# Performance work log

Hardware: AMD Instinct MI355X
Metric: run time of the kernel (lower is better)

Reference implementation:

```python
import jax, jax.numpy as jnp
import numpy as np
import math

IN_FEATURES = 1024
OUT_FEATURES = 1024
N_BANK = 8192
N_LAYER = 12
N_EMBD = 1024


def setup_inputs() -> dict:
    key = jax.random.key(0)
    kq, kk, kv = jax.random.split(key, 3)
    q = jax.random.normal(kq, (4, 2048, IN_FEATURES), dtype=jnp.float32)
    k = 0.02 * jax.random.normal(kk, (N_BANK, IN_FEATURES), dtype=jnp.float32)
    v_std = 2.0 / N_LAYER / math.sqrt(N_EMBD)
    v = v_std * jax.random.normal(kv, (N_BANK, OUT_FEATURES), dtype=jnp.float32)
    return {"q": q, "k": k, "v": v}


def reference(q, k, v):
    # scores: [B, T, N]
    scores = jnp.einsum("btd,nd->btn", q, k)
    # row-wise L2 normalization, scaled by sqrt(N), then exact (erf) GELU
    sqrt_n = jnp.sqrt(jnp.asarray(scores.shape[-1], scores.dtype))
    norm = jnp.linalg.norm(scores, axis=-1, keepdims=True)
    gated = jax.nn.gelu(scores / norm * sqrt_n, approximate=False)
    # out: [B, T, out_features]
    return jnp.einsum("btn,no->bto", gated, v)
```

## Files before the change

### kernel.cpp

```cpp
#include <hip/hip_runtime.h>
#include <hip/hip_bf16.h>
#include <math.h>


#define MROWS 8192
#define DIN   1024
#define NBANK 8192
#define DOUT  1024

typedef float  f32x4  __attribute__((ext_vector_type(4)));
typedef __bf16 bf16x8 __attribute__((ext_vector_type(8)));

__device__ __forceinline__ float bf2f(unsigned short u) {
  union { unsigned int i; float f; } x; x.i = ((unsigned int)u) << 16; return x.f;
}
__device__ __forceinline__ unsigned short f2bf(float f) {
  union { float f; unsigned int i; } x; x.f = f;
  unsigned int u = x.i;
  unsigned int r = (u + 0x7fffu + ((u >> 16) & 1u)) >> 16;
  return (unsigned short)r;
}

__global__ void cvt_kernel(const float* __restrict__ src,
                           unsigned short* __restrict__ dst, int n) {
  int i = (blockIdx.x * 256 + threadIdx.x) * 4;
  if (i >= n) return;
  float4 vv = *(const float4*)(src + i);
  ushort4 o;
  o.x = f2bf(vv.x); o.y = f2bf(vv.y); o.z = f2bf(vv.z); o.w = f2bf(vv.w);
  *(ushort4*)(dst + i) = o;
}

__global__ void transpose_cvt_kernel(const float* __restrict__ src,
                                     unsigned short* __restrict__ dst,
                                     int R, int C) {
  __shared__ float tile[32][33];
  int c0 = blockIdx.x * 32, r0 = blockIdx.y * 32;
  for (int i = threadIdx.y; i < 32; i += 8)
    tile[i][threadIdx.x] = src[(size_t)(r0 + i) * C + c0 + threadIdx.x];
  __syncthreads();
  for (int i = threadIdx.y; i < 32; i += 8)
    dst[(size_t)(c0 + i) * R + r0 + threadIdx.x] = f2bf(tile[threadIdx.x][i]);
}

template <bool OUT_BF16>
__global__ __launch_bounds__(256, 2) void gemm_bt_kernel(
    const unsigned short* __restrict__ A, const unsigned short* __restrict__ B,
    void* __restrict__ C, int K, int ldc) {
  __shared__ unsigned short As[128 * 32];
  __shared__ unsigned short Bs[128 * 32];

  const int tid  = threadIdx.x;
  const int lane = tid & 63;
  const int wave = tid >> 6;
  const int wm   = (wave >> 1) * 64;
  const int wn   = (wave & 1) * 64;
  const int quad = lane >> 4;
  const int l16  = lane & 15;

  const size_t m0 = (size_t)blockIdx.y * 128;
  const size_t n0 = (size_t)blockIdx.x * 128;

  const int srow = tid >> 2;
  const int scol = (tid & 3) * 8;
  const unsigned short* Ag0 = A + (m0 + srow) * (size_t)K + scol;
  const unsigned short* Ag1 = A + (m0 + srow + 64) * (size_t)K + scol;
  const unsigned short* Bg0 = B + (n0 + srow) * (size_t)K + scol;
  const unsigned short* Bg1 = B + (n0 + srow + 64) * (size_t)K + scol;

  unsigned short* AsW0 = As + tid * 8;
  unsigned short* AsW1 = As + 64 * 32 + tid * 8;
  unsigned short* BsW0 = Bs + tid * 8;
  unsigned short* BsW1 = Bs + 64 * 32 + tid * 8;

  const unsigned short* ArP = As + (wm + l16) * 32 + quad * 8;
  const unsigned short* BrP = Bs + (wn + l16) * 32 + quad * 8;

  f32x4 acc[4][4];
#pragma unroll
  for (int i = 0; i < 4; i++)
#pragma unroll
    for (int j = 0; j < 4; j++) {
      f32x4 z = {0.f, 0.f, 0.f, 0.f};
      acc[i][j] = z;
    }

  for (int k0 = 0; k0 < K; k0 += 32) {
    __builtin_amdgcn_global_load_lds(
        (const __attribute__((address_space(1))) unsigned int*)(Ag0 + k0),
        (__attribute__((address_space(3))) unsigned int*)AsW0, 16, 0, 0);
    __builtin_amdgcn_global_load_lds(
        (const __attribute__((address_space(1))) unsigned int*)(Ag1 + k0),
        (__attribute__((address_space(3))) unsigned int*)AsW1, 16, 0, 0);
    __builtin_amdgcn_global_load_lds(
        (const __attribute__((address_space(1))) unsigned int*)(Bg0 + k0),
        (__attribute__((address_space(3))) unsigned int*)BsW0, 16, 0, 0);
    __builtin_amdgcn_global_load_lds(
        (const __attribute__((address_space(1))) unsigned int*)(Bg1 + k0),
        (__attribute__((address_space(3))) unsigned int*)BsW1, 16, 0, 0);
    __syncthreads();

    bf16x8 af[4], bfr[4];
#pragma unroll
    for (int i = 0; i < 4; i++) af[i] = *(const bf16x8*)(ArP + i * 16 * 32);
#pragma unroll
    for (int j = 0; j < 4; j++) bfr[j] = *(const bf16x8*)(BrP + j * 16 * 32);
#pragma unroll
    for (int i = 0; i < 4; i++)
#pragma unroll
      for (int j = 0; j < 4; j++)
        acc[i][j] = __builtin_amdgcn_mfma_f32_16x16x32_bf16(af[i], bfr[j],
                                                            acc[i][j], 0, 0, 0);
    __syncthreads();
  }

#pragma unroll
  for (int i = 0; i < 4; i++)
#pragma unroll
    for (int j = 0; j < 4; j++)
#pragma unroll
      for (int r = 0; r < 4; r++) {
        size_t row = m0 + wm + i * 16 + quad * 4 + r;
        size_t col = n0 + wn + j * 16 + l16;
        float val = acc[i][j][r];
        if (OUT_BF16)
          ((unsigned short*)C)[row * (size_t)ldc + col] = f2bf(val);
        else
          ((float*)C)[row * (size_t)ldc + col] = val;
      }
}

__global__ void rownorm_kernel(const unsigned short* __restrict__ S,
                               float* __restrict__ scale) {
  __shared__ float red[4];
  const int row = blockIdx.x;
  const unsigned short* p = S + (size_t)row * NBANK;
  float sum = 0.f;
  for (int c = threadIdx.x * 8; c < NBANK; c += 256 * 8) {
    uint4 vv = *(const uint4*)(p + c);
    unsigned int w[4] = {vv.x, vv.y, vv.z, vv.w};
#pragma unroll
    for (int e = 0; e < 4; e++) {
      float f0 = bf2f((unsigned short)(w[e] & 0xffffu));
      float f1 = bf2f((unsigned short)(w[e] >> 16));
      sum += f0 * f0 + f1 * f1;
    }
  }
#pragma unroll
  for (int off = 32; off > 0; off >>= 1) sum += __shfl_down(sum, off, 64);
  if ((threadIdx.x & 63) == 0) red[threadIdx.x >> 6] = sum;
  __syncthreads();
  if (threadIdx.x == 0) {
    float t = red[0] + red[1] + red[2] + red[3];
    scale[row] = sqrtf((float)NBANK) / sqrtf(t);
  }
}

__global__ void gelu_kernel(unsigned short* __restrict__ S,
                            const float* __restrict__ scale) {
  size_t idx = ((size_t)blockIdx.x * 256 + threadIdx.x) * 8;
  int row = (int)(idx >> 13);
  float sc = scale[row];
  uint4 vv = *(const uint4*)(S + idx);
  unsigned int w[4] = {vv.x, vv.y, vv.z, vv.w};
#pragma unroll
  for (int e = 0; e < 4; e++) {
    float x0 = bf2f((unsigned short)(w[e] & 0xffffu)) * sc;
    float x1 = bf2f((unsigned short)(w[e] >> 16)) * sc;
    float g0 = 0.5f * x0 * (1.0f + erff(x0 * 0.70710678118654752f));
    float g1 = 0.5f * x1 * (1.0f + erff(x1 * 0.70710678118654752f));
    w[e] = (unsigned int)f2bf(g0) | ((unsigned int)f2bf(g1) << 16);
  }
  uint4 o; o.x = w[0]; o.y = w[1]; o.z = w[2]; o.w = w[3];
  *(uint4*)(S + idx) = o;
}

extern "C" void kernel_launch(void* const* d_in, const int* in_sizes, int n_in,
                              void* d_out, int out_size, void* d_ws, size_t ws_size,
                              hipStream_t stream) {
  const float* q = (const float*)d_in[0];
  const float* k = (const float*)d_in[1];
  const float* v = (const float*)d_in[2];
  float* out = (float*)d_out;

  char* ws = (char*)d_ws;
  const size_t MB = 1024ull * 1024ull;
  unsigned short* qb     = (unsigned short*)(ws);
  unsigned short* kb     = (unsigned short*)(ws + 16 * MB);
  unsigned short* vbT    = (unsigned short*)(ws + 32 * MB);
  unsigned short* scores = (unsigned short*)(ws + 48 * MB);
  float*          scale  = (float*)(ws + 176 * MB);

  const int nqk = MROWS * DIN;

  cvt_kernel<<<nqk / 1024, 256, 0, stream>>>(q, qb, nqk);
  cvt_kernel<<<nqk / 1024, 256, 0, stream>>>(k, kb, nqk);
  transpose_cvt_kernel<<<dim3(DOUT / 32, NBANK / 32), dim3(32, 8), 0, stream>>>(
      v, vbT, NBANK, DOUT);

  gemm_bt_kernel<true><<<dim3(NBANK / 128, MROWS / 128), 256, 0, stream>>>(
      qb, kb, scores, DIN, NBANK);

  rownorm_kernel<<<MROWS, 256, 0, stream>>>(scores, scale);

  gelu_kernel<<<(MROWS * (size_t)NBANK) / (256 * 8), 256, 0, stream>>>(scores, scale);

  gemm_bt_kernel<false><<<dim3(DOUT / 128, MROWS / 128), 256, 0, stream>>>(
      scores, vbT, out, NBANK, DOUT);
}
```

Before: 595.2 us.

## Fuse row sum-of-squares into first GEMM and split-K second GEMM

```diff
diff --git a/kernel.cpp b/kernel.cpp
--- a/kernel.cpp
+++ b/kernel.cpp
@@ -43,12 +43,17 @@
     dst[(size_t)(c0 + i) * R + r0 + threadIdx.x] = f2bf(tile[threadIdx.x][i]);
 }
 
-template <bool OUT_BF16>
-__global__ __launch_bounds__(256, 2) void gemm_bt_kernel(
+__global__ void zero_f32_kernel(float* __restrict__ p, int n4) {
+  int i = blockIdx.x * 256 + threadIdx.x;
+  if (i < n4) ((float4*)p)[i] = make_float4(0.f, 0.f, 0.f, 0.f);
+}
+
+__global__ __launch_bounds__(256, 2) void gemm1_kernel(
     const unsigned short* __restrict__ A, const unsigned short* __restrict__ B,
-    void* __restrict__ C, int K, int ldc) {
+    unsigned short* __restrict__ C, float* __restrict__ sumsq) {
   __shared__ unsigned short As[128 * 32];
   __shared__ unsigned short Bs[128 * 32];
+  const int K = DIN, ldc = NBANK;
 
   const int tid  = threadIdx.x;
   const int lane = tid & 63;
@@ -117,43 +122,26 @@
 #pragma unroll
   for (int i = 0; i < 4; i++)
 #pragma unroll
-    for (int j = 0; j < 4; j++)
-#pragma unroll
-      for (int r = 0; r < 4; r++) {
-        size_t row = m0 + wm + i * 16 + quad * 4 + r;
-        size_t col = n0 + wn + j * 16 + l16;
+    for (int r = 0; r < 4; r++) {
+      size_t row = m0 + wm + i * 16 + quad * 4 + r;
+      float s = 0.f;
+#pragma unroll
+      for (int j = 0; j < 4; j++) {
         float val = acc[i][j][r];
-        if (OUT_BF16)
-          ((unsigned short*)C)[row * (size_t)ldc + col] = f2bf(val);
-        else
-          ((float*)C)[row * (size_t)ldc + col] = val;
+        s += val * val;
+        C[row * (size_t)ldc + n0 + wn + j * 16 + l16] = f2bf(val);
       }
-}
-
-__global__ void rownorm_kernel(const unsigned short* __restrict__ S,
-                               float* __restrict__ scale) {
-  __shared__ float red[4];
-  const int row = blockIdx.x;
-  const unsigned short* p = S + (size_t)row * NBANK;
-  float sum = 0.f;
-  for (int c = threadIdx.x * 8; c < NBANK; c += 256 * 8) {
-    uint4 vv = *(const uint4*)(p + c);
-    unsigned int w[4] = {vv.x, vv.y, vv.z, vv.w};
-#pragma unroll
-    for (int e = 0; e < 4; e++) {
-      float f0 = bf2f((unsigned short)(w[e] & 0xffffu));
-      float f1 = bf2f((unsigned short)(w[e] >> 16));
-      sum += f0 * f0 + f1 * f1;
+      s += __shfl_xor(s, 1);
+      s += __shfl_xor(s, 2);
+      s += __shfl_xor(s, 4);
+      s += __shfl_xor(s, 8);
+      if (l16 == 0) atomicAdd(&sumsq[row], s);
     }
-  }
-#pragma unroll
-  for (int off = 32; off > 0; off >>= 1) sum += __shfl_down(sum, off, 64);
-  if ((threadIdx.x & 63) == 0) red[threadIdx.x >> 6] = sum;
-  __syncthreads();
-  if (threadIdx.x == 0) {
-    float t = red[0] + red[1] + red[2] + red[3];
-    scale[row] = sqrtf((float)NBANK) / sqrtf(t);
-  }
+}
+
+__global__ void finalize_scale_kernel(float* __restrict__ s) {
+  int i = blockIdx.x * 256 + threadIdx.x;
+  if (i < MROWS) s[i] = sqrtf((float)NBANK / s[i]);
 }
 
 __global__ void gelu_kernel(unsigned short* __restrict__ S,
@@ -175,6 +163,86 @@
   *(uint4*)(S + idx) = o;
 }
 
+__global__ __launch_bounds__(512, 4) void gemm2_kernel(
+    const unsigned short* __restrict__ A,
+    const unsigned short* __restrict__ B,
+    float* __restrict__ C) {
+  __shared__ unsigned short As[128 * 32];
+  __shared__ unsigned short Bs[256 * 32];
+  const int K = NBANK, ldc = DOUT;
+
+  const int tid  = threadIdx.x;
+  const int lane = tid & 63;
+  const int wave = tid >> 6;
+  const int wm   = (wave >> 2) * 64;
+  const int wn   = (wave & 3) * 64;
+  const int quad = lane >> 4;
+  const int l16  = lane & 15;
+
+  const size_t m0 = (size_t)blockIdx.y * 128;
+  const size_t n0 = (size_t)blockIdx.x * 256;
+  const int    ks = blockIdx.z * (K / 2);
+
+  const int srow = tid >> 2;
+  const int scol = (tid & 3) * 8;
+  const unsigned short* Ag  = A + (m0 + srow) * (size_t)K + scol + ks;
+  const unsigned short* Bg0 = B + (n0 + srow) * (size_t)K + scol + ks;
+  const unsigned short* Bg1 = B + (n0 + srow + 128) * (size_t)K + scol + ks;
+
+  unsigned short* AsW  = As + tid * 8;
+  unsigned short* BsW0 = Bs + tid * 8;
+  unsigned short* BsW1 = Bs + 512 * 8 + tid * 8;
+
+  const unsigned short* ArP = As + (wm + l16) * 32 + quad * 8;
+  const unsigned short* BrP = Bs + (wn + l16) * 32 + quad * 8;
+
+  f32x4 acc[4][4];
+#pragma unroll
+  for (int i = 0; i < 4; i++)
+#pragma unroll
+    for (int j = 0; j < 4; j++) {
+      f32x4 z = {0.f, 0.f, 0.f, 0.f};
+      acc[i][j] = z;
+    }
+
+  for (int k0 = 0; k0 < K / 2; k0 += 32) {
+    __builtin_amdgcn_global_load_lds(
+        (const __attribute__((address_space(1))) unsigned int*)(Ag + k0),
+        (__attribute__((address_space(3))) unsigned int*)AsW, 16, 0, 0);
+    __builtin_amdgcn_global_load_lds(
+        (const __attribute__((address_space(1))) unsigned int*)(Bg0 + k0),
+        (__attribute__((address_space(3))) unsigned int*)BsW0, 16, 0, 0);
+    __builtin_amdgcn_global_load_lds(
+        (const __attribute__((address_space(1))) unsigned int*)(Bg1 + k0),
+        (__attribute__((address_space(3))) unsigned int*)BsW1, 16, 0, 0);
+    __syncthreads();
+
+    bf16x8 af[4], bfr[4];
+#pragma unroll
+    for (int i = 0; i < 4; i++) af[i] = *(const bf16x8*)(ArP + i * 16 * 32);
+#pragma unroll
+    for (int j = 0; j < 4; j++) bfr[j] = *(const bf16x8*)(BrP + j * 16 * 32);
+#pragma unroll
+    for (int i = 0; i < 4; i++)
+#pragma unroll
+      for (int j = 0; j < 4; j++)
+        acc[i][j] = __builtin_amdgcn_mfma_f32_16x16x32_bf16(af[i], bfr[j],
+                                                            acc[i][j], 0, 0, 0);
+    __syncthreads();
+  }
+
+#pragma unroll
+  for (int i = 0; i < 4; i++)
+#pragma unroll
+    for (int j = 0; j < 4; j++)
+#pragma unroll
+      for (int r = 0; r < 4; r++) {
+        size_t row = m0 + wm + i * 16 + quad * 4 + r;
+        size_t col = n0 + wn + j * 16 + l16;
+        atomicAdd(&C[row * (size_t)ldc + col], acc[i][j][r]);
+      }
+}
+
 extern "C" void kernel_launch(void* const* d_in, const int* in_sizes, int n_in,
                               void* d_out, int out_size, void* d_ws, size_t ws_size,
                               hipStream_t stream) {
@@ -193,18 +261,21 @@
 
   const int nqk = MROWS * DIN;
 
+  zero_f32_kernel<<<(MROWS * DOUT / 4 + 255) / 256, 256, 0, stream>>>(out,
+                                                                      MROWS * DOUT / 4);
+  zero_f32_kernel<<<(MROWS / 4 + 255) / 256, 256, 0, stream>>>(scale, MROWS / 4);
+
   cvt_kernel<<<nqk / 1024, 256, 0, stream>>>(q, qb, nqk);
   cvt_kernel<<<nqk / 1024, 256, 0, stream>>>(k, kb, nqk);
   transpose_cvt_kernel<<<dim3(DOUT / 32, NBANK / 32), dim3(32, 8), 0, stream>>>(
       v, vbT, NBANK, DOUT);
 
-  gemm_bt_kernel<true><<<dim3(NBANK / 128, MROWS / 128), 256, 0, stream>>>(
-      qb, kb, scores, DIN, NBANK);
-
-  rownorm_kernel<<<MROWS, 256, 0, stream>>>(scores, scale);
+  gemm1_kernel<<<dim3(NBANK / 128, MROWS / 128), 256, 0, stream>>>(qb, kb, scores,
+                                                                   scale);
+
+  finalize_scale_kernel<<<MROWS / 256, 256, 0, stream>>>(scale);
 
   gelu_kernel<<<(MROWS * (size_t)NBANK) / (256 * 8), 256, 0, stream>>>(scores, scale);
 
-  gemm_bt_kernel<false><<<dim3(DOUT / 128, MROWS / 128), 256, 0, stream>>>(
-      scores, vbT, out, NBANK, DOUT);
-}
+  gemm2_kernel<<<dim3(DOUT / 256, MROWS / 128, 2), 512, 0, stream>>>(scores, vbT, out);
+}
```

After: 560.0 us. -5.9%, faster.
